# Performance work log

Hardware: AMD Instinct MI355X
Metric: run time of the kernel (lower is better)

Reference implementation:

```python
import jax, jax.numpy as jnp
import numpy as np

NEURONS = 512
CHANNELS = 384
H, W = 13, 13
BATCH = 512


def setup_inputs() -> dict:
    key = jax.random.key(0)
    kx, ks, kd, kb = jax.random.split(key, 4)
    x = jax.random.normal(kx, (BATCH, CHANNELS, H, W), dtype=jnp.float32)
    W_s = jax.random.normal(ks, (NEURONS, H, W), dtype=jnp.float32)      # spatial readout per neuron
    W_d = jax.random.normal(kd, (NEURONS, CHANNELS), dtype=jnp.float32)  # channel readout (squeezed 1x1 conv kernel)
    W_b = jax.random.normal(kb, (1, NEURONS), dtype=jnp.float32)
    return {"x": x, "W_s": W_s, "W_d": W_d, "W_b": W_b}


def reference(x, W_s, W_d, W_b):
    # Original: out = einsum('bchw,nhw->bnchw') -> per-neuron 1x1 conv with W_d[n] -> sum over (c,h,w) -> + W_b
    # Mathematically: out[b,n] = sum_{c,h,w} x[b,c,h,w] * W_s[n,h,w] * W_d[n,c] + W_b[0,n]
    # Factorized into two contractions, avoiding the (b,n,c,h,w) intermediate.
    pooled = jnp.einsum('bchw,nhw->bnc', x, W_s)   # spatial weighted pooling: [B, N, C]
    out = jnp.einsum('bnc,nc->bn', pooled, W_d)    # channel readout: [B, N]
    return out + W_b
```

## Files before the change

### kernel.cpp

```cpp
#include <hip/hip_runtime.h>


#define B_   512
#define C_   384
#define N_   512
#define HW_  169
#define CT   128
#define SXR  200

#define WSF_ELEMS  ((size_t)32 * 6 * 64 * 8)
#define WDF_ELEMS  ((size_t)24 * 32 * 64 * 4)
#define PART_ELEMS ((size_t)3 * B_ * N_)

typedef __bf16 bf16x8 __attribute__((ext_vector_type(8)));
typedef float f32x4  __attribute__((ext_vector_type(4)));
typedef float f32x4u __attribute__((ext_vector_type(4), aligned(4)));
typedef unsigned u32x4 __attribute__((ext_vector_type(4)));

__device__ __forceinline__ __bf16 f2bf(float f) {
  union { float f; unsigned u; } v; v.f = f;
  unsigned r = (v.u + 0x7FFFu + ((v.u >> 16) & 1u)) >> 16;
  unsigned short s = (unsigned short)r;
  return __builtin_bit_cast(__bf16, s);
}

__device__ __forceinline__ unsigned pack_trunc(float a, float b) {
  return __builtin_amdgcn_perm(__builtin_bit_cast(unsigned, b),
                               __builtin_bit_cast(unsigned, a), 0x07060302u);
}

__device__ __forceinline__ void gload_lds16(const __bf16* g, __bf16* l) {
  __builtin_amdgcn_global_load_lds(
      (const __attribute__((address_space(1))) unsigned*)(g),
      (__attribute__((address_space(3))) unsigned*)(l),
      16, 0, 0);
}

__global__ __launch_bounds__(256)
void prep_aux_kernel(const float* __restrict__ Ws,
                     const float* __restrict__ Wd,
                     __bf16* __restrict__ wsf,
                     float* __restrict__ wdf) {
  int t = blockIdx.x * 256 + threadIdx.x;
  if (t < 12288) {
    int lane = t & 63;
    int fr   = t >> 6;
    int kb   = fr % 6;
    int nm   = fr / 6;
    int n    = nm * 16 + (lane & 15);
    int k0   = kb * 32 + (lane >> 4) * 8;
    const float* src = Ws + (size_t)n * HW_;
    bf16x8 v;
    #pragma unroll
    for (int j = 0; j < 8; ++j) {
      int k = k0 + j;
      float f = (k < HW_) ? src[k] : 0.f;
      v[j] = f2bf(f);
    }
    *(bf16x8*)(wsf + (size_t)t * 8) = v;
  } else {
    int t2 = t - 12288;
    int lane = t2 & 63;
    int fr   = t2 >> 6;
    int nm   = fr & 31;
    int cm   = fr >> 5;
    int n    = nm * 16 + (lane & 15);
    int c0   = cm * 16 + (lane >> 4) * 4;
    f32x4 w = *(const f32x4u*)(Wd + (size_t)n * C_ + c0);
    *(f32x4*)(wdf + (size_t)t2 * 4) = w;
  }
}

__global__ __launch_bounds__(256, 4)
void conv_part(const float* __restrict__ x,
               const __bf16* __restrict__ wsf,
               const float* __restrict__ wdf,
               float* __restrict__ part) {
  __shared__ __align__(16) __bf16 Bs[2][12 * 512];
  __shared__ float red[4 * 512];

  const int tid  = threadIdx.x;
  const int id    = blockIdx.x;
  const int slot  = id & 7;
  const int t8    = id >> 3;
  const int c_blk = t8 % 3;
  const int b     = (t8 / 3) * 8 + slot;

  const int lane  = tid & 63;
  const int wv    = tid >> 6;
  const int lrow  = lane & 15;
  const int lquad = lane >> 4;

  bf16x8 a[2][6];
  #pragma unroll
  for (int mi = 0; mi < 2; ++mi) {
    const float* rp = x + ((size_t)b * C_ + (size_t)c_blk * CT + wv * 32 + mi * 16 + lrow) * HW_;
    #pragma unroll
    for (int kb = 0; kb < 6; ++kb) {
      const int k0 = kb * 32 + lquad * 8;
      float v0, v1, v2, v3, v4, v5, v6, v7;
      if (kb < 5 || k0 + 7 < HW_) {
        f32x4u t0 = *(const f32x4u*)(rp + k0);
        f32x4u t1 = *(const f32x4u*)(rp + k0 + 4);
        v0 = t0[0]; v1 = t0[1]; v2 = t0[2]; v3 = t0[3];
        v4 = t1[0]; v5 = t1[1]; v6 = t1[2]; v7 = t1[3];
      } else {
        v0 = (k0 + 0 < HW_) ? rp[k0 + 0] : 0.f;
        v1 = v2 = v3 = v4 = v5 = v6 = v7 = 0.f;
      }
      u32x4 pk;
      pk.x = pack_trunc(v0, v1);
      pk.y = pack_trunc(v2, v3);
      pk.z = pack_trunc(v4, v5);
      pk.w = pack_trunc(v6, v7);
      a[mi][kb] = __builtin_bit_cast(bf16x8, pk);
    }
  }

  const int cm0 = c_blk * 8 + wv * 2;
  const float* wb = wdf + (size_t)lane * 4;
  const f32x4 zero = {0.f, 0.f, 0.f, 0.f};
  float* rbase = red + wv * 512;

  {
    const __bf16* g = wsf + ((size_t)(wv * 3) * 512) + (size_t)lane * 8;
    __bf16* l = &Bs[0][(wv * 3) * 512];
    #pragma unroll
    for (int j = 0; j < 3; ++j)
      gload_lds16(g + j * 512, l + j * 512);
  }
  __syncthreads();

  #pragma unroll 1
  for (int ch = 0; ch < 16; ++ch) {
    const int buf = ch & 1;

    f32x4 w[2][2];
    #pragma unroll
    for (int nfi = 0; nfi < 2; ++nfi)
      #pragma unroll
      for (int mi = 0; mi < 2; ++mi)
        w[nfi][mi] = *(const f32x4*)(wb +
            (((size_t)(cm0 + mi) * 32 + (ch * 2 + nfi)) * 256));

    if (ch < 15) {
      const __bf16* g = wsf + ((size_t)((ch + 1) * 12 + wv * 3) * 512) + (size_t)lane * 8;
      __bf16* l = &Bs[buf ^ 1][(wv * 3) * 512];
      #pragma unroll
      for (int j = 0; j < 3; ++j)
        gload_lds16(g + j * 512, l + j * 512);
    }

    #pragma unroll
    for (int nfi = 0; nfi < 2; ++nfi) {
      f32x4 acc[2] = {zero, zero};
      #pragma unroll
      for (int kb = 0; kb < 6; ++kb) {
        const bf16x8 bfr = *(const bf16x8*)&Bs[buf][(nfi * 6 + kb) * 512 + lane * 8];
        acc[0] = __builtin_amdgcn_mfma_f32_16x16x32_bf16(a[0][kb], bfr, acc[0], 0, 0, 0);
        acc[1] = __builtin_amdgcn_mfma_f32_16x16x32_bf16(a[1][kb], bfr, acc[1], 0, 0, 0);
      }

      float t = 0.f;
      #pragma unroll
      for (int mi = 0; mi < 2; ++mi)
        t += acc[mi][0] * w[nfi][mi][0] + acc[mi][1] * w[nfi][mi][1]
           + acc[mi][2] * w[nfi][mi][2] + acc[mi][3] * w[nfi][mi][3];
      t += __shfl_xor(t, 16, 64);
      t += __shfl_xor(t, 32, 64);
      if (lane < 16)
        rbase[(ch * 2 + nfi) * 16 + lrow] = t;
    }

    __syncthreads();
  }

  float* pb = part + ((size_t)c_blk * B_ + b) * N_;
  #pragma unroll
  for (int r = 0; r < 2; ++r) {
    const int n = r * 256 + tid;
    float v = red[n] + red[512 + n] + red[1024 + n] + red[1536 + n];
    pb[n] = v;
  }
}

__global__ __launch_bounds__(256)
void reduce_part(const float* __restrict__ part,
                 const float* __restrict__ Wb,
                 float* __restrict__ out) {
  const size_t S = (size_t)B_ * N_;
  int idx = (blockIdx.x * 256 + threadIdx.x) * 4;
  f32x4 a0 = *(const f32x4u*)(part + idx);
  f32x4 a1 = *(const f32x4u*)(part + S + idx);
  f32x4 a2 = *(const f32x4u*)(part + 2 * S + idx);
  f32x4 wb = *(const f32x4u*)(Wb + (idx & (N_ - 1)));
  f32x4 r;
  #pragma unroll
  for (int i = 0; i < 4; ++i)
    r[i] = a0[i] + a1[i] + a2[i] + wb[i];
  *(f32x4*)(out + idx) = r;
}

__global__ __launch_bounds__(256, 3)
void conv_fused_v8(const float* __restrict__ x,
                   const __bf16* __restrict__ wsf,
                   const float* __restrict__ wdf,
                   const float* __restrict__ Wb,
                   float* __restrict__ out) {
  __shared__ __align__(16) __bf16 Xs[CT * SXR];
  __shared__ float red[4][64];

  const int tid  = threadIdx.x;
  const int id    = blockIdx.x;
  const int slot  = id & 7;
  const int t8    = id >> 3;
  const int c_blk = t8 % 3;
  const int b     = (t8 / 3) * 8 + slot;

  const int lane  = tid & 63;
  const int wv    = tid >> 6;
  const int cq    = (wv >> 1) * 64;
  const int nq    = (wv & 1) * 64;
  const int lrow  = lane & 15;
  const int lquad = lane >> 4;

  const float* src = x + ((size_t)b * C_ + (size_t)c_blk * CT) * HW_;
  #pragma unroll 4
  for (int p = 0; p < 24; ++p) {
    int i   = p * 256 + tid;
    int row = i / 48;
    int ch  = i - row * 48;
    const float* bp = src + row * HW_ + ch * 4;
    float v0 = 0.f, v1 = 0.f, v2 = 0.f, v3 = 0.f;
    if (ch < 42) {
      f32x4u t = *(const f32x4u*)bp;
      v0 = t[0]; v1 = t[1]; v2 = t[2]; v3 = t[3];
    } else if (ch == 42) {
      v0 = bp[0];
    }
    unsigned d0 = pack_trunc(v0, v1);
    unsigned d1 = pack_trunc(v2, v3);
    uint2 d; d.x = d0; d.y = d1;
    *(uint2*)&Xs[row * SXR + ch * 4] = d;
  }
  __syncthreads();

  const int cm0 = c_blk * 8 + (cq >> 4);

  #pragma unroll 1
  for (int nb = 0; nb < 4; ++nb) {
    const int nm0 = nb * 8 + (nq >> 4);
    const __bf16* bbase = wsf + ((size_t)nm0 * 6) * 512 + (size_t)lane * 8;

    const f32x4 zero = {0.f, 0.f, 0.f, 0.f};
    f32x4 acc[4][4];
    #pragma unroll
    for (int mi = 0; mi < 4; ++mi)
      #pragma unroll
      for (int ni = 0; ni < 4; ++ni)
        acc[mi][ni] = zero;

    #pragma unroll
    for (int kb = 0; kb < 6; ++kb) {
      bf16x8 afr[4], bfr[4];
      #pragma unroll
      for (int mi = 0; mi < 4; ++mi)
        afr[mi] = *(const bf16x8*)&Xs[(cq + mi * 16 + lrow) * SXR + kb * 32 + lquad * 8];
      #pragma unroll
      for (int ni = 0; ni < 4; ++ni)
        bfr[ni] = *(const bf16x8*)(bbase + ((size_t)ni * 6 + kb) * 512);
      #pragma unroll
      for (int mi = 0; mi < 4; ++mi)
        #pragma unroll
        for (int ni = 0; ni < 4; ++ni)
          acc[mi][ni] = __builtin_amdgcn_mfma_f32_16x16x32_bf16(
              afr[mi], bfr[ni], acc[mi][ni], 0, 0, 0);
    }

    float s[4] = {0.f, 0.f, 0.f, 0.f};
    #pragma unroll
    for (int ni = 0; ni < 4; ++ni) {
      #pragma unroll
      for (int mi = 0; mi < 4; ++mi) {
        const f32x4 w = *(const f32x4*)(wdf +
            (((size_t)(cm0 + mi) * 32 + (nm0 + ni)) * 64 + lane) * 4);
        s[ni] += acc[mi][ni][0] * w[0] + acc[mi][ni][1] * w[1]
               + acc[mi][ni][2] * w[2] + acc[mi][ni][3] * w[3];
      }
    }

    #pragma unroll
    for (int ni = 0; ni < 4; ++ni) {
      s[ni] += __shfl_xor(s[ni], 16, 64);
      s[ni] += __shfl_xor(s[ni], 32, 64);
    }
    if (lane < 16) {
      #pragma unroll
      for (int ni = 0; ni < 4; ++ni)
        red[wv][ni * 16 + lrow] = s[ni];
    }
    __syncthreads();

    if (tid < 128) {
      const int half = tid >> 6;
      const int idx  = tid & 63;
      const int n    = nb * 128 + tid;
      float v = red[half][idx] + red[half + 2][idx];
      if (c_blk == 0) v += Wb[n];
      atomicAdd(&out[(size_t)b * N_ + n], v);
    }
    __syncthreads();
  }
}


#define LDSS 104
#define KCH  96
#define NT   128

__global__ __launch_bounds__(256)
void conv_main_fallback(const float* __restrict__ x,
                        const float* __restrict__ Ws_g,
                        const float* __restrict__ Wd,
                        const float* __restrict__ Wb,
                        float* __restrict__ out) {
  __shared__ __align__(16) __bf16 Xs[CT][LDSS];
  __shared__ __align__(16) __bf16 Ws[NT][LDSS];

  const int tid   = threadIdx.x;
  const int n_blk = blockIdx.x;
  const int c_blk = blockIdx.y;
  const int b     = blockIdx.z;
  const int c0 = c_blk * CT;
  const int n0 = n_blk * NT;
  const int lane  = tid & 63;
  const int wv    = tid >> 6;
  const int cq    = (wv >> 1) * 64;
  const int nq    = (wv & 1) * 64;
  const int lrow  = lane & 15;
  const int lquad = lane >> 4;

  const f32x4 zero = {0.f, 0.f, 0.f, 0.f};
  f32x4 acc[4][4];
  #pragma unroll
  for (int mi = 0; mi < 4; ++mi)
    #pragma unroll
    for (int ni = 0; ni < 4; ++ni)
      acc[mi][ni] = zero;

  const float* xb  = x    + (size_t)b  * (C_ * HW_) + (size_t)c0 * HW_;
  const float* wsb = Ws_g + (size_t)n0 * HW_;

  for (int ch = 0; ch < 2; ++ch) {
    const int k0 = ch * KCH;
    __syncthreads();
    for (int e = tid; e < CT * KCH; e += 256) {
      int r   = e / KCH;
      int col = e - r * KCH;
      int k   = k0 + col;
      float vx = 0.f, vw = 0.f;
      if (k < HW_) {
        vx = xb [r * HW_ + k];
        vw = wsb[r * HW_ + k];
      }
      Xs[r][col] = f2bf(vx);
      Ws[r][col] = f2bf(vw);
    }
    __syncthreads();

    #pragma unroll
    for (int ks = 0; ks < 3; ++ks) {
      const int kc = ks * 32 + lquad * 8;
      bf16x8 afr[4], bfr[4];
      #pragma unroll
      for (int mi = 0; mi < 4; ++mi)
        afr[mi] = *(const bf16x8*)&Xs[cq + mi * 16 + lrow][kc];
      #pragma unroll
      for (int ni = 0; ni < 4; ++ni)
        bfr[ni] = *(const bf16x8*)&Ws[nq + ni * 16 + lrow][kc];
      #pragma unroll
      for (int mi = 0; mi < 4; ++mi)
        #pragma unroll
        for (int ni = 0; ni < 4; ++ni)
          acc[mi][ni] = __builtin_amdgcn_mfma_f32_16x16x32_bf16(
              afr[mi], bfr[ni], acc[mi][ni], 0, 0, 0);
    }
  }

  #pragma unroll
  for (int ni = 0; ni < 4; ++ni) {
    const int n = n0 + nq + ni * 16 + lrow;
    float sv = 0.f;
    #pragma unroll
    for (int mi = 0; mi < 4; ++mi) {
      const int cbase = c0 + cq + mi * 16 + lquad * 4;
      #pragma unroll
      for (int i = 0; i < 4; ++i)
        sv += acc[mi][ni][i] * Wd[(size_t)n * C_ + (cbase + i)];
    }
    sv += __shfl_xor(sv, 16, 64);
    sv += __shfl_xor(sv, 32, 64);
    if (lane < 16) {
      if (c_blk == 0 && cq == 0) sv += Wb[n];
      atomicAdd(&out[(size_t)b * N_ + n], sv);
    }
  }
}

extern "C" void kernel_launch(void* const* d_in, const int* in_sizes, int n_in,
                              void* d_out, int out_size, void* d_ws, size_t ws_size,
                              hipStream_t stream) {
  const float* x   = (const float*)d_in[0];
  const float* Wsp = (const float*)d_in[1];
  const float* Wd  = (const float*)d_in[2];
  const float* Wb  = (const float*)d_in[3];
  float* out = (float*)d_out;

  const size_t need_basic = WSF_ELEMS * sizeof(__bf16) + WDF_ELEMS * sizeof(float);
  const size_t need_full  = need_basic + PART_ELEMS * sizeof(float);

  if (ws_size >= need_full) {
    __bf16* wsf  = (__bf16*)d_ws;
    float*  wdf  = (float*)(wsf + WSF_ELEMS);
    float*  partb = wdf + WDF_ELEMS;

    prep_aux_kernel<<<240, 256, 0, stream>>>(Wsp, Wd, wsf, wdf);
    conv_part<<<1536, 256, 0, stream>>>(x, wsf, wdf, partb);
    reduce_part<<<256, 256, 0, stream>>>(partb, Wb, out);
  } else if (ws_size >= need_basic) {
    __bf16* wsf = (__bf16*)d_ws;
    float*  wdf = (float*)(wsf + WSF_ELEMS);

    hipMemsetAsync(d_out, 0, (size_t)out_size * sizeof(float), stream);
    prep_aux_kernel<<<240, 256, 0, stream>>>(Wsp, Wd, wsf, wdf);
    conv_fused_v8<<<1536, 256, 0, stream>>>(x, wsf, wdf, Wb, out);
  } else {
    hipMemsetAsync(d_out, 0, (size_t)out_size * sizeof(float), stream);
    dim3 grid(N_ / NT, C_ / CT, B_);
    conv_main_fallback<<<grid, 256, 0, stream>>>(x, Wsp, Wd, Wb, out);
  }
}
```

Baseline: 225.0 us.

## Process two batch rows per block to reuse staged spatial weights

Each conv_part block now loads and converts x for two batch rows and runs MFMAs for both against the same LDS-staged spatial weight tiles, halving the grid and the per-output weight streaming. LDS reduction buffers double and register pressure rises, so the launch bound drops to 3 waves per SIMD. An explicit vmem wait is added before each barrier so the asynchronous global-to-LDS loads are complete before use.

```diff
diff --git a/kernel.cpp b/kernel.cpp
--- a/kernel.cpp
+++ b/kernel.cpp
@@ -34,6 +34,10 @@
       (const __attribute__((address_space(1))) unsigned*)(g),
       (__attribute__((address_space(3))) unsigned*)(l),
       16, 0, 0);
+}
+
+__device__ __forceinline__ void drain_vmem() {
+  asm volatile("s_waitcnt vmcnt(0)" ::: "memory");
 }
 
 __global__ __launch_bounds__(256)
@@ -71,56 +75,60 @@
   }
 }
 
-__global__ __launch_bounds__(256, 4)
+__global__ __launch_bounds__(256, 3)
 void conv_part(const float* __restrict__ x,
                const __bf16* __restrict__ wsf,
                const float* __restrict__ wdf,
                float* __restrict__ part) {
   __shared__ __align__(16) __bf16 Bs[2][12 * 512];
-  __shared__ float red[4 * 512];
+  __shared__ float red[2][4 * 512];
 
   const int tid  = threadIdx.x;
   const int id    = blockIdx.x;
   const int slot  = id & 7;
   const int t8    = id >> 3;
   const int c_blk = t8 % 3;
-  const int b     = (t8 / 3) * 8 + slot;
+  const int bp    = (t8 / 3) * 8 + slot;
+  const int b0    = bp * 2;
 
   const int lane  = tid & 63;
   const int wv    = tid >> 6;
   const int lrow  = lane & 15;
   const int lquad = lane >> 4;
 
-  bf16x8 a[2][6];
+  bf16x8 a[2][2][6];
   #pragma unroll
-  for (int mi = 0; mi < 2; ++mi) {
-    const float* rp = x + ((size_t)b * C_ + (size_t)c_blk * CT + wv * 32 + mi * 16 + lrow) * HW_;
-    #pragma unroll
-    for (int kb = 0; kb < 6; ++kb) {
-      const int k0 = kb * 32 + lquad * 8;
-      float v0, v1, v2, v3, v4, v5, v6, v7;
-      if (kb < 5 || k0 + 7 < HW_) {
-        f32x4u t0 = *(const f32x4u*)(rp + k0);
-        f32x4u t1 = *(const f32x4u*)(rp + k0 + 4);
-        v0 = t0[0]; v1 = t0[1]; v2 = t0[2]; v3 = t0[3];
-        v4 = t1[0]; v5 = t1[1]; v6 = t1[2]; v7 = t1[3];
-      } else {
-        v0 = (k0 + 0 < HW_) ? rp[k0 + 0] : 0.f;
-        v1 = v2 = v3 = v4 = v5 = v6 = v7 = 0.f;
+  for (int bi = 0; bi < 2; ++bi) {
+    #pragma unroll
+    for (int mi = 0; mi < 2; ++mi) {
+      const float* rp = x + ((size_t)(b0 + bi) * C_ + (size_t)c_blk * CT
+                             + wv * 32 + mi * 16 + lrow) * HW_;
+      #pragma unroll
+      for (int kb = 0; kb < 6; ++kb) {
+        const int k0 = kb * 32 + lquad * 8;
+        float v0, v1, v2, v3, v4, v5, v6, v7;
+        if (kb < 5 || k0 + 7 < HW_) {
+          f32x4u t0 = *(const f32x4u*)(rp + k0);
+          f32x4u t1 = *(const f32x4u*)(rp + k0 + 4);
+          v0 = t0[0]; v1 = t0[1]; v2 = t0[2]; v3 = t0[3];
+          v4 = t1[0]; v5 = t1[1]; v6 = t1[2]; v7 = t1[3];
+        } else {
+          v0 = (k0 + 0 < HW_) ? rp[k0 + 0] : 0.f;
+          v1 = v2 = v3 = v4 = v5 = v6 = v7 = 0.f;
+        }
+        u32x4 pk;
+        pk.x = pack_trunc(v0, v1);
+        pk.y = pack_trunc(v2, v3);
+        pk.z = pack_trunc(v4, v5);
+        pk.w = pack_trunc(v6, v7);
+        a[bi][mi][kb] = __builtin_bit_cast(bf16x8, pk);
       }
-      u32x4 pk;
-      pk.x = pack_trunc(v0, v1);
-      pk.y = pack_trunc(v2, v3);
-      pk.z = pack_trunc(v4, v5);
-      pk.w = pack_trunc(v6, v7);
-      a[mi][kb] = __builtin_bit_cast(bf16x8, pk);
     }
   }
 
   const int cm0 = c_blk * 8 + wv * 2;
   const float* wb = wdf + (size_t)lane * 4;
   const f32x4 zero = {0.f, 0.f, 0.f, 0.f};
-  float* rbase = red + wv * 512;
 
   {
     const __bf16* g = wsf + ((size_t)(wv * 3) * 512) + (size_t)lane * 8;
@@ -129,6 +137,7 @@
     for (int j = 0; j < 3; ++j)
       gload_lds16(g + j * 512, l + j * 512);
   }
+  drain_vmem();
   __syncthreads();
 
   #pragma unroll 1
@@ -153,34 +162,45 @@
 
     #pragma unroll
     for (int nfi = 0; nfi < 2; ++nfi) {
-      f32x4 acc[2] = {zero, zero};
+      f32x4 acc[2][2] = {{zero, zero}, {zero, zero}};
       #pragma unroll
       for (int kb = 0; kb < 6; ++kb) {
         const bf16x8 bfr = *(const bf16x8*)&Bs[buf][(nfi * 6 + kb) * 512 + lane * 8];
-        acc[0] = __builtin_amdgcn_mfma_f32_16x16x32_bf16(a[0][kb], bfr, acc[0], 0, 0, 0);
-        acc[1] = __builtin_amdgcn_mfma_f32_16x16x32_bf16(a[1][kb], bfr, acc[1], 0, 0, 0);
+        #pragma unroll
+        for (int bi = 0; bi < 2; ++bi) {
+          acc[bi][0] = __builtin_amdgcn_mfma_f32_16x16x32_bf16(a[bi][0][kb], bfr, acc[bi][0], 0, 0, 0);
+          acc[bi][1] = __builtin_amdgcn_mfma_f32_16x16x32_bf16(a[bi][1][kb], bfr, acc[bi][1], 0, 0, 0);
+        }
       }
 
-      float t = 0.f;
-      #pragma unroll
-      for (int mi = 0; mi < 2; ++mi)
-        t += acc[mi][0] * w[nfi][mi][0] + acc[mi][1] * w[nfi][mi][1]
-           + acc[mi][2] * w[nfi][mi][2] + acc[mi][3] * w[nfi][mi][3];
-      t += __shfl_xor(t, 16, 64);
-      t += __shfl_xor(t, 32, 64);
-      if (lane < 16)
-        rbase[(ch * 2 + nfi) * 16 + lrow] = t;
-    }
-
+      #pragma unroll
+      for (int bi = 0; bi < 2; ++bi) {
+        float t = 0.f;
+        #pragma unroll
+        for (int mi = 0; mi < 2; ++mi)
+          t += acc[bi][mi][0] * w[nfi][mi][0] + acc[bi][mi][1] * w[nfi][mi][1]
+             + acc[bi][mi][2] * w[nfi][mi][2] + acc[bi][mi][3] * w[nfi][mi][3];
+        t += __shfl_xor(t, 16, 64);
+        t += __shfl_xor(t, 32, 64);
+        if (lane < 16)
+          red[bi][wv * 512 + (ch * 2 + nfi) * 16 + lrow] = t;
+      }
+    }
+
+    drain_vmem();
     __syncthreads();
   }
 
-  float* pb = part + ((size_t)c_blk * B_ + b) * N_;
+  float* pb = part + ((size_t)c_blk * B_ + b0) * N_;
   #pragma unroll
   for (int r = 0; r < 2; ++r) {
     const int n = r * 256 + tid;
-    float v = red[n] + red[512 + n] + red[1024 + n] + red[1536 + n];
-    pb[n] = v;
+    #pragma unroll
+    for (int bi = 0; bi < 2; ++bi) {
+      const float* rb = red[bi];
+      float v = rb[n] + rb[512 + n] + rb[1024 + n] + rb[1536 + n];
+      pb[(size_t)bi * N_ + n] = v;
+    }
   }
 }
 
@@ -425,7 +445,7 @@
     float*  partb = wdf + WDF_ELEMS;
 
     prep_aux_kernel<<<240, 256, 0, stream>>>(Wsp, Wd, wsf, wdf);
-    conv_part<<<1536, 256, 0, stream>>>(x, wsf, wdf, partb);
+    conv_part<<<768, 256, 0, stream>>>(x, wsf, wdf, partb);
     reduce_part<<<256, 256, 0, stream>>>(partb, Wb, out);
   } else if (ws_size >= need_basic) {
     __bf16* wsf = (__bf16*)d_ws;
```

After: 238.4 us. 1.06x slower.
